# Kernel tuning notes

Hardware: AMD Instinct MI355X
Metric: run time of the kernel (lower is better)

The kernel has to match this reference:

```python
import jax, jax.numpy as jnp
import numpy as np

B, S, D = 1, 2048, 4096
H, KV, HD = 32, 8, 128          # n_heads, n_kv_heads, head_dim
NREP = H // KV                  # 4
SCALE = 1.0 / np.sqrt(HD).astype(np.float32)
ROPE_THETA = 10000.0


def setup_inputs() -> dict:
    key = jax.random.key(0)
    kx, kq, kk, kv, ko = jax.random.split(key, 5)
    x = jax.random.normal(kx, (B, S, D), jnp.float32)
    # precomputed rotary embeddings: (S, HD//2, 2) = (cos, sin)
    inv_freq = 1.0 / (ROPE_THETA ** (np.arange(0, HD, 2, dtype=np.float64) / HD))
    ang = np.outer(np.arange(S, dtype=np.float64), inv_freq)
    freqs_cis = jnp.asarray(np.stack([np.cos(ang), np.sin(ang)], axis=-1), jnp.float32)
    # additive causal mask
    mask = jnp.triu(jnp.full((S, S), -1e9, jnp.float32), k=1)
    std = 0.02
    wq = jax.random.normal(kq, (H * HD, D), jnp.float32) * std   # torch Linear layout (out, in)
    wk = jax.random.normal(kk, (KV * HD, D), jnp.float32) * std
    wv = jax.random.normal(kv, (KV * HD, D), jnp.float32) * std
    wo = jax.random.normal(ko, (D, H * HD), jnp.float32) * std
    return {"x": x, "freqs_cis": freqs_cis, "mask": mask,
            "wq": wq, "wk": wk, "wv": wv, "wo": wo}


def _apply_rope(t, fc):
    # t: [B, S, h, HD]; fc: [S, HD//2, 2] (cos, sin). Pairs adjacent dims as complex.
    b, s, h, hd = t.shape
    tr = t.reshape(b, s, h, hd // 2, 2)
    cos = fc[None, :, None, :, 0]
    sin = fc[None, :, None, :, 1]
    re = tr[..., 0] * cos - tr[..., 1] * sin
    im = tr[..., 0] * sin + tr[..., 1] * cos
    return jnp.stack([re, im], axis=-1).reshape(b, s, h, hd)


def reference(x, freqs_cis, mask, wq, wk, wv, wo):
    q = (x @ wq.T).reshape(B, S, H, HD)
    k = (x @ wk.T).reshape(B, S, KV, HD)
    v = (x @ wv.T).reshape(B, S, KV, HD)
    q = _apply_rope(q, freqs_cis)
    k = _apply_rope(k, freqs_cis)
    # GQA: head h = g * NREP + r attends to kv group g (same math as repeat_kv)
    qg = q.reshape(B, S, KV, NREP, HD)
    scores = jnp.einsum('bsgrd,btgd->bgrst', qg, k) * SCALE  # [B,KV,NREP,S,S]
    scores = scores + mask
    probs = jax.nn.softmax(scores.astype(jnp.float32), axis=-1).astype(q.dtype)
    out = jnp.einsum('bgrst,btgd->bsgrd', probs, v).reshape(B, S, H * HD)
    return out @ wo.T
```

## Files before the change

kernel.cpp:

```cpp
#include <hip/hip_runtime.h>
#include <stdint.h>

#define SCALE_F 0.08838834764831845f
#define LOG2E_F 1.4426950408889634f

typedef __bf16 bf16x8_t __attribute__((ext_vector_type(8)));
typedef unsigned short u16x8 __attribute__((ext_vector_type(8)));
typedef float f32x4 __attribute__((ext_vector_type(4)));
typedef float f32x16 __attribute__((ext_vector_type(16)));

__device__ __forceinline__ unsigned short f2bf(float f) {
  unsigned int u = __float_as_uint(f);
  unsigned int r = ((u >> 16) & 1u) + 0x7FFFu;
  return (unsigned short)((u + r) >> 16);
}
__device__ __forceinline__ float bf2f(unsigned short s) {
  return __uint_as_float(((unsigned int)s) << 16);
}
__device__ __forceinline__ f32x4 mfma16(u16x8 a, u16x8 b, f32x4 c) {
  return __builtin_amdgcn_mfma_f32_16x16x32_bf16(
      __builtin_bit_cast(bf16x8_t, a), __builtin_bit_cast(bf16x8_t, b), c, 0, 0, 0);
}
__device__ __forceinline__ f32x16 mfma32(u16x8 a, u16x8 b, f32x16 c) {
  return __builtin_amdgcn_mfma_f32_32x32x16_bf16(
      __builtin_bit_cast(bf16x8_t, a), __builtin_bit_cast(bf16x8_t, b), c, 0, 0, 0);
}
__device__ __forceinline__ unsigned int cvtpk(float lo, float hi) {
  unsigned int r;
  asm("v_cvt_pk_bf16_f32 %0, %1, %2" : "=v"(r) : "v"(lo), "v"(hi));
  return r;
}
__device__ __forceinline__ float exp2_hw(float x) {
  float r;
  asm("v_exp_f32 %0, %1" : "=v"(r) : "v"(x));
  return r;
}
__device__ __forceinline__ void gload_lds16(const void* g, void* l) {
  __builtin_amdgcn_global_load_lds((const __attribute__((address_space(1))) void*)g,
                                   (__attribute__((address_space(3))) void*)l, 16, 0, 0);
}

__global__ void cvtk(const float* __restrict__ in, unsigned short* __restrict__ out, int n) {
  int i = (blockIdx.x * blockDim.x + threadIdx.x) * 4;
  if (i >= n) return;
  float4 v = *(const float4*)(in + i);
  unsigned int p0 = (unsigned int)f2bf(v.x) | ((unsigned int)f2bf(v.y) << 16);
  unsigned int p1 = (unsigned int)f2bf(v.z) | ((unsigned int)f2bf(v.w) << 16);
  *(uint2*)(out + i) = make_uint2(p0, p1);
}

__global__ void ropek(unsigned short* __restrict__ buf, const float* __restrict__ fc,
                      int hshift, int rowstride, float scale) {
  int idx = blockIdx.x * blockDim.x + threadIdx.x;
  int j = idx & 63;
  int h = (idx >> 6) & ((1 << hshift) - 1);
  int s = idx >> (6 + hshift);
  unsigned short* p = buf + (size_t)s * rowstride + h * 128 + 2 * j;
  float cs = fc[(s * 64 + j) * 2];
  float sn = fc[(s * 64 + j) * 2 + 1];
  float a = bf2f(p[0]), b = bf2f(p[1]);
  unsigned int o0 = f2bf((a * cs - b * sn) * scale);
  unsigned int o1 = f2bf((a * sn + b * cs) * scale);
  *(unsigned int*)p = o0 | (o1 << 16);
}

__global__ void ktile(const unsigned short* __restrict__ QKV, const float* __restrict__ fc,
                      unsigned short* __restrict__ Ktil) {
  int b = blockIdx.x;
  int kvg = b >> 6, kvt = b & 63;
  int tid = threadIdx.x;
#pragma unroll
  for (int cc = 0; cc < 2; ++cc) {
    int c = tid + cc * 256;
    int s = c >> 5, r = c & 31;
    int key = kvt * 32 + r;
    u16x8 v = *(const u16x8*)&QKV[(size_t)key * 6144 + 4096 + kvg * 128 + s * 8];
    unsigned int o[4];
#pragma unroll
    for (int t = 0; t < 4; ++t) {
      int m = s * 4 + t;
      float cs = fc[(key * 64 + m) * 2];
      float sn = fc[(key * 64 + m) * 2 + 1];
      float a = bf2f((unsigned short)v[2 * t]), bb = bf2f((unsigned short)v[2 * t + 1]);
      o[t] = (unsigned int)f2bf(a * cs - bb * sn) | ((unsigned int)f2bf(a * sn + bb * cs) << 16);
    }
    *(uint4*)&Ktil[(size_t)b * 4096 + c * 8] = make_uint4(o[0], o[1], o[2], o[3]);
  }
}

__global__ void vtile(const unsigned short* __restrict__ QKV, unsigned short* __restrict__ Vtil) {
  int b = blockIdx.x;
  int kvg = b >> 6, kvt = b & 63;
  int tid = threadIdx.x;
#pragma unroll
  for (int cc = 0; cc < 2; ++cc) {
    int c = tid + cc * 256;
    int v = c >> 7, hd = c & 127;
    unsigned short o[8];
#pragma unroll
    for (int t = 0; t < 8; ++t)
      o[t] = QKV[(size_t)(kvt * 32 + v * 8 + t) * 6144 + 5120 + kvg * 128 + hd];
    *(uint4*)&Vtil[(size_t)b * 4096 + c * 8] = *(uint4*)o;
  }
}

__global__ __launch_bounds__(512, 2) void gemm_qkv(const unsigned short* __restrict__ A,
                                                   const unsigned short* __restrict__ BT,
                                                   unsigned short* __restrict__ C) {
  const int K = 4096, N = 6144;
  __shared__ __align__(16) unsigned short smem[2 * 28672];
  const int tid = threadIdx.x;
  const int w = tid >> 6, l = tid & 63;
  const int wm = w >> 2, wn = w & 3;
  const int c16 = l & 15, h4 = l >> 4;
  const int wg = ((int)blockIdx.x & 7) * 32 + ((int)blockIdx.x >> 3);
  const int m0 = (wg & 7) << 8, n0 = (wg >> 3) * 192;

  int growA[4], gcolA[4], growB[3], gcolB[3];
#pragma unroll
  for (int p = 0; p < 4; ++p) {
    int c = p * 512 + tid, ll = c & 63;
    growA[p] = ((c >> 6) & 15) * 16 + (ll & 15);
    gcolA[p] = (c >> 10) * 32 + ((ll >> 4) << 3);
  }
#pragma unroll
  for (int p = 0; p < 3; ++p) {
    int c = p * 512 + tid, ll = c & 63, f6 = c >> 6;
    int kc = (f6 >= 12) ? 1 : 0;
    growB[p] = (f6 - 12 * kc) * 16 + (ll & 15);
    gcolB[p] = kc * 32 + ((ll >> 4) << 3);
  }
  auto stageA = [&](int e, int ks, int p) {
    gload_lds16(A + (size_t)(m0 + growA[p]) * K + ks + gcolA[p],
                &smem[e * 28672 + (p * 512 + tid) * 8]);
  };
  auto stageB = [&](int e, int ks, int p) {
    gload_lds16(BT + (size_t)(n0 + growB[p]) * K + ks + gcolB[p],
                &smem[e * 28672 + 16384 + (p * 512 + tid) * 8]);
  };

  f32x4 acc[2][4][3];
#pragma unroll
  for (int mh = 0; mh < 2; ++mh)
#pragma unroll
    for (int mf = 0; mf < 4; ++mf)
#pragma unroll
      for (int nf = 0; nf < 3; ++nf)
#pragma unroll
        for (int r = 0; r < 4; ++r) acc[mh][mf][nf][r] = 0.f;

  stageA(0, 0, 0); stageA(0, 0, 1); stageB(0, 0, 0); stageB(0, 0, 1);
  stageA(0, 0, 2); stageA(0, 0, 3); stageB(0, 0, 2);
  asm volatile("s_waitcnt vmcnt(3)" ::: "memory");
  __builtin_amdgcn_sched_barrier(0);
  asm volatile("s_barrier" ::: "memory");

  const int nt = K >> 6;
  u16x8 bfr[3];
  for (int t = 0; t < nt; ++t) {
    const int d = t & 1, e = d ^ 1;
    const int dA = d * 28672, dB = dA + 16384;
    const int ks = ((t + 1 < nt) ? t + 1 : t) << 6;
#pragma unroll
    for (int p = 0; p < 4; ++p) {
      const int kc = p >> 1, mh = p & 1;
      u16x8 af[4];
#pragma unroll
      for (int mf = 0; mf < 4; ++mf)
        af[mf] = *(const u16x8*)&smem[dA + ((kc * 16 + wm * 8 + mh * 4 + mf) * 64 + l) * 8];
      if (mh == 0) {
#pragma unroll
        for (int nf = 0; nf < 3; ++nf)
          bfr[nf] = *(const u16x8*)&smem[dB + ((kc * 12 + wn * 3 + nf) * 64 + l) * 8];
      }
      if (p == 0)      { stageA(e, ks, 0); stageA(e, ks, 1); }
      else if (p == 1) { stageB(e, ks, 0); stageB(e, ks, 1); }
      else if (p == 2) { stageA(e, ks, 2); stageA(e, ks, 3); }
      else             { stageB(e, ks, 2); }
      asm volatile("s_barrier" ::: "memory");
      asm volatile("s_waitcnt lgkmcnt(0)" ::: "memory");
      __builtin_amdgcn_sched_barrier(0);
      __builtin_amdgcn_s_setprio(1);
#pragma unroll
      for (int mf = 0; mf < 4; ++mf)
#pragma unroll
        for (int nf = 0; nf < 3; ++nf)
          acc[mh][mf][nf] = mfma16(af[mf], bfr[nf], acc[mh][mf][nf]);
      __builtin_amdgcn_s_setprio(0);
      __builtin_amdgcn_sched_barrier(0);
      if (p == 1) asm volatile("s_waitcnt vmcnt(4)" ::: "memory");
      else if (p == 3) asm volatile("s_waitcnt vmcnt(3)" ::: "memory");
      asm volatile("s_barrier" ::: "memory");
    }
  }
  asm volatile("s_waitcnt vmcnt(0)" ::: "memory");

#pragma unroll
  for (int mh = 0; mh < 2; ++mh)
#pragma unroll
    for (int mf = 0; mf < 4; ++mf)
#pragma unroll
      for (int nf = 0; nf < 3; ++nf)
#pragma unroll
        for (int r = 0; r < 4; ++r) {
          int row = m0 + wm * 128 + mh * 64 + mf * 16 + h4 * 4 + r;
          int col = n0 + wn * 48 + nf * 16 + c16;
          C[(size_t)row * N + col] = f2bf(acc[mh][mf][nf][r]);
        }
}

__global__ __launch_bounds__(512, 2) void gemm_o(const unsigned short* __restrict__ A,
                                                 const unsigned short* __restrict__ BT,
                                                 float* __restrict__ C) {
  const int K = 4096, N = 4096;
  __shared__ __align__(16) unsigned short smem[2 * 24576];
  const int tid = threadIdx.x;
  const int w = tid >> 6, l = tid & 63;
  const int wm = w >> 2, wn = w & 3;
  const int c16 = l & 15, h4 = l >> 4;
  const int wg = ((int)blockIdx.x & 7) * 32 + ((int)blockIdx.x >> 3);
  const int m0 = (wg & 15) << 7, n0 = (wg >> 4) << 8;

  int growA[2], gcolA[2], growB[4], gcolB[4];
#pragma unroll
  for (int p = 0; p < 2; ++p) {
    int c = p * 512 + tid, ll = c & 63;
    growA[p] = ((c >> 6) & 7) * 16 + (ll & 15);
    gcolA[p] = (c >> 9) * 32 + ((ll >> 4) << 3);
  }
#pragma unroll
  for (int p = 0; p < 4; ++p) {
    int c = p * 512 + tid, ll = c & 63;
    growB[p] = ((c >> 6) & 15) * 16 + (ll & 15);
    gcolB[p] = (c >> 10) * 32 + ((ll >> 4) << 3);
  }
  auto stageA = [&](int e, int ks, int p) {
    gload_lds16(A + (size_t)(m0 + growA[p]) * K + ks + gcolA[p],
                &smem[e * 24576 + (p * 512 + tid) * 8]);
  };
  auto stageB = [&](int e, int ks, int p) {
    gload_lds16(BT + (size_t)(n0 + growB[p]) * K + ks + gcolB[p],
                &smem[e * 24576 + 8192 + (p * 512 + tid) * 8]);
  };

  f32x4 acc[4][4];
#pragma unroll
  for (int mf = 0; mf < 4; ++mf)
#pragma unroll
    for (int nc = 0; nc < 4; ++nc)
#pragma unroll
      for (int r = 0; r < 4; ++r) acc[mf][nc][r] = 0.f;

  stageA(0, 0, 0); stageB(0, 0, 0); stageB(0, 0, 1);
  stageA(0, 0, 1); stageB(0, 0, 2); stageB(0, 0, 3);
  asm volatile("s_waitcnt vmcnt(3)" ::: "memory");
  __builtin_amdgcn_sched_barrier(0);
  asm volatile("s_barrier" ::: "memory");

  const int nt = K >> 6;
  u16x8 af[4];
  for (int t = 0; t < nt; ++t) {
    const int d = t & 1, e = d ^ 1;
    const int dA = d * 24576, dB = dA + 8192;
    const int ks = ((t + 1 < nt) ? t + 1 : t) << 6;
#pragma unroll
    for (int p = 0; p < 4; ++p) {
      const int kc = p >> 1, nh = p & 1;
      if (nh == 0) {
#pragma unroll
        for (int mf = 0; mf < 4; ++mf)
          af[mf] = *(const u16x8*)&smem[dA + ((kc * 8 + wm * 4 + mf) * 64 + l) * 8];
      }
      u16x8 bfr[2];
#pragma unroll
      for (int nf = 0; nf < 2; ++nf)
        bfr[nf] = *(const u16x8*)&smem[dB + ((kc * 16 + wn * 4 + nh * 2 + nf) * 64 + l) * 8];
      if (p == 0)      { stageA(e, ks, 0); stageB(e, ks, 0); }
      else if (p == 1) { stageB(e, ks, 1); }
      else if (p == 2) { stageA(e, ks, 1); stageB(e, ks, 2); }
      else             { stageB(e, ks, 3); }
      asm volatile("s_barrier" ::: "memory");
      asm volatile("s_waitcnt lgkmcnt(0)" ::: "memory");
      __builtin_amdgcn_sched_barrier(0);
      __builtin_amdgcn_s_setprio(1);
#pragma unroll
      for (int mf = 0; mf < 4; ++mf)
#pragma unroll
        for (int nf = 0; nf < 2; ++nf)
          acc[mf][nh * 2 + nf] = mfma16(af[mf], bfr[nf], acc[mf][nh * 2 + nf]);
      __builtin_amdgcn_s_setprio(0);
      __builtin_amdgcn_sched_barrier(0);
      if (p == 1 || p == 3) asm volatile("s_waitcnt vmcnt(3)" ::: "memory");
      asm volatile("s_barrier" ::: "memory");
    }
  }
  asm volatile("s_waitcnt vmcnt(0)" ::: "memory");

#pragma unroll
  for (int mf = 0; mf < 4; ++mf)
#pragma unroll
    for (int nc = 0; nc < 4; ++nc)
#pragma unroll
      for (int r = 0; r < 4; ++r) {
        int row = m0 + wm * 64 + mf * 16 + h4 * 4 + r;
        int col = n0 + wn * 64 + nc * 16 + c16;
        C[(size_t)row * N + col] = acc[mf][nc][r];
      }
}

__global__ __launch_bounds__(256) void attnk(const unsigned short* __restrict__ Q,
                                             const unsigned short* __restrict__ Ktil,
                                             const unsigned short* __restrict__ Vtil,
                                             unsigned short* __restrict__ Ao) {
  __shared__ __align__(16) unsigned short Kbuf[2][4096];
  __shared__ __align__(16) unsigned short Vbuf[2][4096];
  const int tid = threadIdx.x;
  const int w = tid >> 6, l = tid & 63;
  const int q31 = l & 31, hi = l >> 5;
  const int b = blockIdx.x;
  const int kvg = b & 7;
  const int qg = 63 - (b >> 3);
  const int head = kvg * 4 + w;
  const int qrow = qg * 32 + q31;

  u16x8 qf[8];
#pragma unroll
  for (int kc = 0; kc < 8; ++kc)
    qf[kc] = *(const u16x8*)&Q[(size_t)qrow * 6144 + head * 128 + kc * 16 + hi * 8];

  f32x16 accO[4];
#pragma unroll
  for (int f = 0; f < 4; ++f)
#pragma unroll
    for (int r = 0; r < 16; ++r) accO[f][r] = 0.f;
  float m_run = -1e30f, l_run = 0.f;

  const unsigned short* ktb = Ktil + (size_t)kvg * 64 * 4096;
  const unsigned short* vtb = Vtil + (size_t)kvg * 64 * 4096;
  auto STAGE = [&](int d, int t) {
    const unsigned short* ks = ktb + (size_t)t * 4096 + w * 1024 + l * 8;
    const unsigned short* vs = vtb + (size_t)t * 4096 + w * 1024 + l * 8;
    gload_lds16(ks, &Kbuf[d][w * 1024 + l * 8]);
    gload_lds16(ks + 512, &Kbuf[d][w * 1024 + 512 + l * 8]);
    gload_lds16(vs, &Vbuf[d][w * 1024 + l * 8]);
    gload_lds16(vs + 512, &Vbuf[d][w * 1024 + 512 + l * 8]);
  };

  STAGE(0, 0);
  int cur = 0;
  for (int kvt = 0; kvt <= qg; ++kvt) {
    __builtin_amdgcn_s_barrier();
    __builtin_amdgcn_sched_barrier(0);
    if (kvt < qg) {
      STAGE(cur ^ 1, kvt + 1);
      asm volatile("s_waitcnt vmcnt(4)" ::: "memory");
    } else {
      asm volatile("s_waitcnt vmcnt(0)" ::: "memory");
    }
    __builtin_amdgcn_s_barrier();
    __builtin_amdgcn_sched_barrier(0);

    f32x16 s;
#pragma unroll
    for (int r = 0; r < 16; ++r) s[r] = 0.f;
#pragma unroll
    for (int kc = 0; kc < 8; ++kc) {
      u16x8 kf = *(const u16x8*)&Kbuf[cur][((2 * kc + hi) * 32 + q31) * 8];
      s = mfma32(kf, qf[kc], s);
    }

    if (kvt == qg) {
#pragma unroll
      for (int r = 0; r < 16; ++r) {
        int key = (r & 3) + 8 * (r >> 2) + 4 * hi;
        if (key > q31) s[r] = -1e30f;
      }
    }

    float pm = s[0];
#pragma unroll
    for (int r = 1; r < 16; ++r) pm = fmaxf(pm, s[r]);
    pm = fmaxf(pm, __shfl_xor(pm, 32, 64));
    if (!__all(pm - m_run <= 8.f)) {
      float mn = fmaxf(m_run, pm);
      float al = exp2_hw(m_run - mn);
      m_run = mn;
      l_run *= al;
#pragma unroll
      for (int f = 0; f < 4; ++f)
#pragma unroll
        for (int r = 0; r < 16; ++r) accO[f][r] *= al;
    }
    float p[16], ls = 0.f;
#pragma unroll
    for (int r = 0; r < 16; ++r) { p[r] = exp2_hw(s[r] - m_run); ls += p[r]; }
    l_run += ls + __shfl_xor(ls, 32, 64);

    unsigned int wv[8], wp[8];
#pragma unroll
    for (int i = 0; i < 8; ++i) wv[i] = cvtpk(p[2 * i], p[2 * i + 1]);
#pragma unroll
    for (int i = 0; i < 8; ++i) wp[i] = (unsigned int)__shfl_xor((int)wv[i], 32, 64);
    union { unsigned int u[4]; u16x8 v; } pf0, pf1;
    pf0.u[0] = hi ? wp[2] : wv[0];
    pf0.u[1] = hi ? wp[3] : wv[1];
    pf0.u[2] = hi ? wv[2] : wp[0];
    pf0.u[3] = hi ? wv[3] : wp[1];
    pf1.u[0] = hi ? wp[6] : wv[4];
    pf1.u[1] = hi ? wp[7] : wv[5];
    pf1.u[2] = hi ? wv[6] : wp[4];
    pf1.u[3] = hi ? wv[7] : wp[5];

#pragma unroll
    for (int f = 0; f < 4; ++f) {
      u16x8 vf0 = *(const u16x8*)&Vbuf[cur][((hi) * 128 + f * 32 + q31) * 8];
      u16x8 vf1 = *(const u16x8*)&Vbuf[cur][((2 + hi) * 128 + f * 32 + q31) * 8];
      accO[f] = mfma32(vf0, pf0.v, accO[f]);
      accO[f] = mfma32(vf1, pf1.v, accO[f]);
    }
    cur ^= 1;
  }

  float linv = 1.0f / l_run;
  unsigned short* orow = Ao + (size_t)qrow * 4096 + head * 128;
#pragma unroll
  for (int f = 0; f < 4; ++f)
#pragma unroll
    for (int g4 = 0; g4 < 4; ++g4) {
      unsigned int lo = (unsigned int)f2bf(accO[f][g4 * 4 + 0] * linv) |
                        ((unsigned int)f2bf(accO[f][g4 * 4 + 1] * linv) << 16);
      unsigned int hi2 = (unsigned int)f2bf(accO[f][g4 * 4 + 2] * linv) |
                         ((unsigned int)f2bf(accO[f][g4 * 4 + 3] * linv) << 16);
      *(uint2*)(orow + f * 32 + 8 * g4 + 4 * hi) = make_uint2(lo, hi2);
    }
}

extern "C" void kernel_launch(void* const* d_in, const int* in_sizes, int n_in,
                              void* d_out, int out_size, void* d_ws, size_t ws_size,
                              hipStream_t stream) {
  (void)in_sizes; (void)n_in; (void)out_size; (void)ws_size;
  const float* x  = (const float*)d_in[0];
  const float* fc = (const float*)d_in[1];
  const float* wq = (const float*)d_in[3];
  const float* wk = (const float*)d_in[4];
  const float* wv = (const float*)d_in[5];
  const float* wo = (const float*)d_in[6];

  const size_t M = 1024 * 1024;
  unsigned short* xb   = (unsigned short*)d_ws;
  unsigned short* wfus = xb   + 8 * M;
  unsigned short* wob  = wfus + 24 * M;
  unsigned short* QKV  = wob  + 16 * M;
  unsigned short* Ktil = QKV  + 12 * M;
  unsigned short* Vtil = Ktil + 2 * M;
  unsigned short* Ab   = xb;

  cvtk<<<dim3(8 * M / 1024), 256, 0, stream>>>(x, xb, 8 * M);
  cvtk<<<dim3(16 * M / 1024), 256, 0, stream>>>(wq, wfus, 16 * M);
  cvtk<<<dim3(4 * M / 1024), 256, 0, stream>>>(wk, wfus + 16 * M, 4 * M);
  cvtk<<<dim3(4 * M / 1024), 256, 0, stream>>>(wv, wfus + 20 * M, 4 * M);
  cvtk<<<dim3(16 * M / 1024), 256, 0, stream>>>(wo, wob, 16 * M);

  gemm_qkv<<<dim3(256), 512, 0, stream>>>(xb, wfus, QKV);

  ropek<<<dim3(2048 * 32 * 64 / 256), 256, 0, stream>>>(QKV, fc, 5, 6144, SCALE_F * LOG2E_F);
  ktile<<<dim3(512), 256, 0, stream>>>(QKV, fc, Ktil);
  vtile<<<dim3(512), 256, 0, stream>>>(QKV, Vtil);

  attnk<<<dim3(512), 256, 0, stream>>>(QKV, Ktil, Vtil, Ab);

  gemm_o<<<dim3(256), 512, 0, stream>>>(Ab, wob, (float*)d_out);
}
```

Measured before the change: 367.5 us.

## Fuse RoPE into QKV GEMM epilogue and simplify GEMM pipelining

Applies rotary embedding and Q scaling in the QKV GEMM epilogue using lane shuffles to pair adjacent columns, removing the separate ropek pass and the RoPE math in ktile. The GEMM main loops in gemm_qkv and gemm_o are restructured to issue all next-tile prefetches up front, use fewer barriers per tile, and wait for all loads at the end of each iteration. This cuts an extra memory pass over Q/K but may reduce load/compute overlap in the GEMMs.

```diff
diff --git a/kernel.cpp b/kernel.cpp
--- a/kernel.cpp
+++ b/kernel.cpp
@@ -3,6 +3,7 @@
 
 #define SCALE_F 0.08838834764831845f
 #define LOG2E_F 1.4426950408889634f
+#define QS_F (SCALE_F * LOG2E_F)
 
 typedef __bf16 bf16x8_t __attribute__((ext_vector_type(8)));
 typedef unsigned short u16x8 __attribute__((ext_vector_type(8)));
@@ -49,23 +50,7 @@
   *(uint2*)(out + i) = make_uint2(p0, p1);
 }
 
-__global__ void ropek(unsigned short* __restrict__ buf, const float* __restrict__ fc,
-                      int hshift, int rowstride, float scale) {
-  int idx = blockIdx.x * blockDim.x + threadIdx.x;
-  int j = idx & 63;
-  int h = (idx >> 6) & ((1 << hshift) - 1);
-  int s = idx >> (6 + hshift);
-  unsigned short* p = buf + (size_t)s * rowstride + h * 128 + 2 * j;
-  float cs = fc[(s * 64 + j) * 2];
-  float sn = fc[(s * 64 + j) * 2 + 1];
-  float a = bf2f(p[0]), b = bf2f(p[1]);
-  unsigned int o0 = f2bf((a * cs - b * sn) * scale);
-  unsigned int o1 = f2bf((a * sn + b * cs) * scale);
-  *(unsigned int*)p = o0 | (o1 << 16);
-}
-
-__global__ void ktile(const unsigned short* __restrict__ QKV, const float* __restrict__ fc,
-                      unsigned short* __restrict__ Ktil) {
+__global__ void ktile(const unsigned short* __restrict__ QKV, unsigned short* __restrict__ Ktil) {
   int b = blockIdx.x;
   int kvg = b >> 6, kvt = b & 63;
   int tid = threadIdx.x;
@@ -74,17 +59,8 @@
     int c = tid + cc * 256;
     int s = c >> 5, r = c & 31;
     int key = kvt * 32 + r;
-    u16x8 v = *(const u16x8*)&QKV[(size_t)key * 6144 + 4096 + kvg * 128 + s * 8];
-    unsigned int o[4];
-#pragma unroll
-    for (int t = 0; t < 4; ++t) {
-      int m = s * 4 + t;
-      float cs = fc[(key * 64 + m) * 2];
-      float sn = fc[(key * 64 + m) * 2 + 1];
-      float a = bf2f((unsigned short)v[2 * t]), bb = bf2f((unsigned short)v[2 * t + 1]);
-      o[t] = (unsigned int)f2bf(a * cs - bb * sn) | ((unsigned int)f2bf(a * sn + bb * cs) << 16);
-    }
-    *(uint4*)&Ktil[(size_t)b * 4096 + c * 8] = make_uint4(o[0], o[1], o[2], o[3]);
+    *(uint4*)&Ktil[(size_t)b * 4096 + c * 8] =
+        *(const uint4*)&QKV[(size_t)key * 6144 + 4096 + kvg * 128 + s * 8];
   }
 }
 
@@ -106,6 +82,7 @@
 
 __global__ __launch_bounds__(512, 2) void gemm_qkv(const unsigned short* __restrict__ A,
                                                    const unsigned short* __restrict__ BT,
+                                                   const float* __restrict__ fc,
                                                    unsigned short* __restrict__ C) {
   const int K = 4096, N = 6144;
   __shared__ __align__(16) unsigned short smem[2 * 28672];
@@ -149,64 +126,86 @@
 #pragma unroll
         for (int r = 0; r < 4; ++r) acc[mh][mf][nf][r] = 0.f;
 
-  stageA(0, 0, 0); stageA(0, 0, 1); stageB(0, 0, 0); stageB(0, 0, 1);
-  stageA(0, 0, 2); stageA(0, 0, 3); stageB(0, 0, 2);
-  asm volatile("s_waitcnt vmcnt(3)" ::: "memory");
+  stageA(0, 0, 0); stageA(0, 0, 1); stageA(0, 0, 2); stageA(0, 0, 3);
+  stageB(0, 0, 0); stageB(0, 0, 1); stageB(0, 0, 2);
+  asm volatile("s_waitcnt vmcnt(0)" ::: "memory");
   __builtin_amdgcn_sched_barrier(0);
   asm volatile("s_barrier" ::: "memory");
 
   const int nt = K >> 6;
-  u16x8 bfr[3];
   for (int t = 0; t < nt; ++t) {
     const int d = t & 1, e = d ^ 1;
     const int dA = d * 28672, dB = dA + 16384;
     const int ks = ((t + 1 < nt) ? t + 1 : t) << 6;
-#pragma unroll
-    for (int p = 0; p < 4; ++p) {
-      const int kc = p >> 1, mh = p & 1;
-      u16x8 af[4];
-#pragma unroll
-      for (int mf = 0; mf < 4; ++mf)
-        af[mf] = *(const u16x8*)&smem[dA + ((kc * 16 + wm * 8 + mh * 4 + mf) * 64 + l) * 8];
-      if (mh == 0) {
+    stageA(e, ks, 0); stageA(e, ks, 1); stageA(e, ks, 2); stageA(e, ks, 3);
+    stageB(e, ks, 0); stageB(e, ks, 1); stageB(e, ks, 2);
+    u16x8 af[2][4], bfr[2][3];
+#pragma unroll
+    for (int kc = 0; kc < 2; ++kc) {
+#pragma unroll
+      for (int mf = 0; mf < 4; ++mf)
+        af[kc][mf] = *(const u16x8*)&smem[dA + ((kc * 16 + wm * 8 + mf) * 64 + l) * 8];
+#pragma unroll
+      for (int nf = 0; nf < 3; ++nf)
+        bfr[kc][nf] = *(const u16x8*)&smem[dB + ((kc * 12 + wn * 3 + nf) * 64 + l) * 8];
+    }
+    asm volatile("s_barrier" ::: "memory");
+    asm volatile("s_waitcnt lgkmcnt(0)" ::: "memory");
+    __builtin_amdgcn_sched_barrier(0);
+    __builtin_amdgcn_s_setprio(1);
+#pragma unroll
+    for (int kc = 0; kc < 2; ++kc)
+#pragma unroll
+      for (int mf = 0; mf < 4; ++mf)
 #pragma unroll
         for (int nf = 0; nf < 3; ++nf)
-          bfr[nf] = *(const u16x8*)&smem[dB + ((kc * 12 + wn * 3 + nf) * 64 + l) * 8];
-      }
-      if (p == 0)      { stageA(e, ks, 0); stageA(e, ks, 1); }
-      else if (p == 1) { stageB(e, ks, 0); stageB(e, ks, 1); }
-      else if (p == 2) { stageA(e, ks, 2); stageA(e, ks, 3); }
-      else             { stageB(e, ks, 2); }
-      asm volatile("s_barrier" ::: "memory");
-      asm volatile("s_waitcnt lgkmcnt(0)" ::: "memory");
-      __builtin_amdgcn_sched_barrier(0);
-      __builtin_amdgcn_s_setprio(1);
+          acc[0][mf][nf] = mfma16(af[kc][mf], bfr[kc][nf], acc[0][mf][nf]);
+    __builtin_amdgcn_s_setprio(0);
+    __builtin_amdgcn_sched_barrier(0);
+    asm volatile("s_barrier" ::: "memory");
+    u16x8 af2[2][4];
+#pragma unroll
+    for (int kc = 0; kc < 2; ++kc)
+#pragma unroll
+      for (int mf = 0; mf < 4; ++mf)
+        af2[kc][mf] = *(const u16x8*)&smem[dA + ((kc * 16 + wm * 8 + 4 + mf) * 64 + l) * 8];
+    asm volatile("s_waitcnt lgkmcnt(0)" ::: "memory");
+    __builtin_amdgcn_sched_barrier(0);
+    __builtin_amdgcn_s_setprio(1);
+#pragma unroll
+    for (int kc = 0; kc < 2; ++kc)
 #pragma unroll
       for (int mf = 0; mf < 4; ++mf)
 #pragma unroll
         for (int nf = 0; nf < 3; ++nf)
-          acc[mh][mf][nf] = mfma16(af[mf], bfr[nf], acc[mh][mf][nf]);
-      __builtin_amdgcn_s_setprio(0);
-      __builtin_amdgcn_sched_barrier(0);
-      if (p == 1) asm volatile("s_waitcnt vmcnt(4)" ::: "memory");
-      else if (p == 3) asm volatile("s_waitcnt vmcnt(3)" ::: "memory");
-      asm volatile("s_barrier" ::: "memory");
-    }
-  }
-  asm volatile("s_waitcnt vmcnt(0)" ::: "memory");
+          acc[1][mf][nf] = mfma16(af2[kc][mf], bfr[kc][nf], acc[1][mf][nf]);
+    __builtin_amdgcn_s_setprio(0);
+    __builtin_amdgcn_sched_barrier(0);
+    asm volatile("s_waitcnt vmcnt(0)" ::: "memory");
+    asm volatile("s_barrier" ::: "memory");
+  }
 
 #pragma unroll
   for (int mh = 0; mh < 2; ++mh)
 #pragma unroll
     for (int mf = 0; mf < 4; ++mf)
 #pragma unroll
-      for (int nf = 0; nf < 3; ++nf)
+      for (int nf = 0; nf < 3; ++nf) {
+        const int colbase = n0 + wn * 48 + nf * 16;
 #pragma unroll
         for (int r = 0; r < 4; ++r) {
           int row = m0 + wm * 128 + mh * 64 + mf * 16 + h4 * 4 + r;
-          int col = n0 + wn * 48 + nf * 16 + c16;
-          C[(size_t)row * N + col] = f2bf(acc[mh][mf][nf][r]);
+          float v = acc[mh][mf][nf][r];
+          if (colbase < 5120) {
+            float other = __shfl_xor(v, 1, 64);
+            int j = ((colbase & 127) >> 1) + (c16 >> 1);
+            float2 csn = *(const float2*)&fc[((size_t)row * 64 + j) * 2];
+            float o = (c16 & 1) ? (other * csn.y + v * csn.x) : (v * csn.x - other * csn.y);
+            v = (colbase < 4096) ? o * QS_F : o;
+          }
+          C[(size_t)row * N + colbase + c16] = f2bf(v);
         }
+      }
 }
 
 __global__ __launch_bounds__(512, 2) void gemm_o(const unsigned short* __restrict__ A,
@@ -251,50 +250,44 @@
 #pragma unroll
       for (int r = 0; r < 4; ++r) acc[mf][nc][r] = 0.f;
 
-  stageA(0, 0, 0); stageB(0, 0, 0); stageB(0, 0, 1);
-  stageA(0, 0, 1); stageB(0, 0, 2); stageB(0, 0, 3);
-  asm volatile("s_waitcnt vmcnt(3)" ::: "memory");
+  stageA(0, 0, 0); stageA(0, 0, 1);
+  stageB(0, 0, 0); stageB(0, 0, 1); stageB(0, 0, 2); stageB(0, 0, 3);
+  asm volatile("s_waitcnt vmcnt(0)" ::: "memory");
   __builtin_amdgcn_sched_barrier(0);
   asm volatile("s_barrier" ::: "memory");
 
   const int nt = K >> 6;
-  u16x8 af[4];
   for (int t = 0; t < nt; ++t) {
     const int d = t & 1, e = d ^ 1;
     const int dA = d * 24576, dB = dA + 8192;
     const int ks = ((t + 1 < nt) ? t + 1 : t) << 6;
-#pragma unroll
-    for (int p = 0; p < 4; ++p) {
-      const int kc = p >> 1, nh = p & 1;
-      if (nh == 0) {
-#pragma unroll
-        for (int mf = 0; mf < 4; ++mf)
-          af[mf] = *(const u16x8*)&smem[dA + ((kc * 8 + wm * 4 + mf) * 64 + l) * 8];
-      }
-      u16x8 bfr[2];
-#pragma unroll
-      for (int nf = 0; nf < 2; ++nf)
-        bfr[nf] = *(const u16x8*)&smem[dB + ((kc * 16 + wn * 4 + nh * 2 + nf) * 64 + l) * 8];
-      if (p == 0)      { stageA(e, ks, 0); stageB(e, ks, 0); }
-      else if (p == 1) { stageB(e, ks, 1); }
-      else if (p == 2) { stageA(e, ks, 1); stageB(e, ks, 2); }
-      else             { stageB(e, ks, 3); }
-      asm volatile("s_barrier" ::: "memory");
+    stageA(e, ks, 0); stageA(e, ks, 1);
+    stageB(e, ks, 0); stageB(e, ks, 1); stageB(e, ks, 2); stageB(e, ks, 3);
+#pragma unroll
+    for (int kc = 0; kc < 2; ++kc) {
+      u16x8 af[4], bfr[4];
+#pragma unroll
+      for (int mf = 0; mf < 4; ++mf)
+        af[mf] = *(const u16x8*)&smem[dA + ((kc * 8 + wm * 4 + mf) * 64 + l) * 8];
+#pragma unroll
+      for (int nc = 0; nc < 4; ++nc)
+        bfr[nc] = *(const u16x8*)&smem[dB + ((kc * 16 + wn * 4 + nc) * 64 + l) * 8];
+      if (kc == 0) asm volatile("s_barrier" ::: "memory");
       asm volatile("s_waitcnt lgkmcnt(0)" ::: "memory");
       __builtin_amdgcn_sched_barrier(0);
       __builtin_amdgcn_s_setprio(1);
 #pragma unroll
       for (int mf = 0; mf < 4; ++mf)
 #pragma unroll
-        for (int nf = 0; nf < 2; ++nf)
-          acc[mf][nh * 2 + nf] = mfma16(af[mf], bfr[nf], acc[mf][nh * 2 + nf]);
+        for (int nc = 0; nc < 4; ++nc)
+          acc[mf][nc] = mfma16(af[mf], bfr[nc], acc[mf][nc]);
       __builtin_amdgcn_s_setprio(0);
       __builtin_amdgcn_sched_barrier(0);
-      if (p == 1 || p == 3) asm volatile("s_waitcnt vmcnt(3)" ::: "memory");
-      asm volatile("s_barrier" ::: "memory");
-    }
-  }
-  asm volatile("s_waitcnt vmcnt(0)" ::: "memory");
+      if (kc == 0) asm volatile("s_barrier" ::: "memory");
+    }
+    asm volatile("s_waitcnt vmcnt(0)" ::: "memory");
+    asm volatile("s_barrier" ::: "memory");
+  }
 
 #pragma unroll
   for (int mf = 0; mf < 4; ++mf)
@@ -461,10 +454,9 @@
   cvtk<<<dim3(4 * M / 1024), 256, 0, stream>>>(wv, wfus + 20 * M, 4 * M);
   cvtk<<<dim3(16 * M / 1024), 256, 0, stream>>>(wo, wob, 16 * M);
 
-  gemm_qkv<<<dim3(256), 512, 0, stream>>>(xb, wfus, QKV);
-
-  ropek<<<dim3(2048 * 32 * 64 / 256), 256, 0, stream>>>(QKV, fc, 5, 6144, SCALE_F * LOG2E_F);
-  ktile<<<dim3(512), 256, 0, stream>>>(QKV, fc, Ktil);
+  gemm_qkv<<<dim3(256), 512, 0, stream>>>(xb, wfus, fc, QKV);
+
+  ktile<<<dim3(512), 256, 0, stream>>>(QKV, Ktil);
   vtile<<<dim3(512), 256, 0, stream>>>(QKV, Vtil);
 
   attnk<<<dim3(512), 256, 0, stream>>>(QKV, Ktil, Vtil, Ab);
```

Result: slower. 424.8 us (+15.6%).
